# Optimization experiments

Measured on AMD Instinct MI355X. Metric: run time of the kernel, lower is better.

Reference implementation:

```python
import jax, jax.numpy as jnp
import numpy as np

EPSILON = 0.5

def setup_inputs() -> dict:
    key = jax.random.key(0)
    k1, k2, k3 = jax.random.split(key, 3)
    N, F, D = 8192, 128, 64
    X = jax.random.normal(k1, (N, F), dtype=jnp.float32)
    W_r = jax.random.normal(k2, (2 * F, D), dtype=jnp.float32)
    a_r = jax.random.normal(k3, (D,), dtype=jnp.float32)
    return {"X": X, "W_r": W_r, "a_r": a_r}

def reference(X, W_r, a_r):
    # Faithful to: cat(X_i, X_j) @ W_r @ a_r == (X @ W1 @ a_r)[i] + (X @ W2 @ a_r)[j]
    # (standard GAT decomposition -- avoids materializing [N, N, 2F]).
    F_ = X.shape[1]
    w1 = W_r[:F_] @ a_r          # [F]
    w2 = W_r[F_:] @ a_r          # [F]
    s1 = X @ w1                  # [N]
    s2 = X @ w2                  # [N]
    R = jax.nn.leaky_relu(s1[:, None] + s2[None, :])   # [N, N]
    # torch .std() is unbiased (ddof=1) over all elements
    R = (R - R.mean()) / (jnp.std(R, ddof=1) + 1e-5)
    E = jax.nn.softmax(R, axis=1)
    threshold = E.mean() / EPSILON
    filtered_E = jnp.where(E >= threshold, jnp.float32(1.0), jnp.float32(0.0))
    return filtered_E
```

## Files before the change

kernel.cpp:

```cpp
#include <hip/hip_runtime.h>
#include <math.h>

#define Nn 8192

static constexpr int S1o = 256;
static constexpr int S2o = S1o + Nn;
static constexpr int Mo  = S2o + Nn;
static constexpr int Zo  = Mo + Nn;
static constexpr int RRo = Zo + Nn;
static constexpr int STo = RRo + Nn;
static constexpr int RBo = STo + 8;

typedef float nfloat4 __attribute__((ext_vector_type(4)));

__device__ __forceinline__ float lrelu32(float z) {
    return (z >= 0.0f) ? z : __fmul_rn(0.01f, z);
}

__device__ __forceinline__ double exp_fast(double x) {
    x = fmin(fmax(x, -700.0), 700.0);
    const double INVLN2 = 1.44269504088896338700e+00;
    const double LN2HI  = 6.93147180369123816490e-01;
    const double LN2LO  = 1.90821492927058770002e-10;
    double nd = rint(x * INVLN2);
    double r  = fma(-nd, LN2HI, x);
    r = fma(-nd, LN2LO, r);
    double p = 1.56192069685862264622e-10;
    p = fma(p, r, 2.08767569878680989792e-09);
    p = fma(p, r, 2.50521083854417187751e-08);
    p = fma(p, r, 2.75573192239858906526e-07);
    p = fma(p, r, 2.75573192239858925110e-06);
    p = fma(p, r, 2.48015873015873015873e-05);
    p = fma(p, r, 1.98412698412698412698e-04);
    p = fma(p, r, 1.38888888888888894069e-03);
    p = fma(p, r, 8.33333333333333321769e-03);
    p = fma(p, r, 4.16666666666666643537e-02);
    p = fma(p, r, 1.66666666666666657415e-01);
    p = fma(p, r, 5.00000000000000000000e-01);
    p = fma(p, r, 1.0);
    p = fma(p, r, 1.0);
    long long n = (long long)nd;
    double sc = __longlong_as_double((n + 1023LL) << 52);
    return p * sc;
}
__device__ __forceinline__ float exp32cr(float x) {
    return (float)exp_fast((double)x);
}

__device__ float blas_dot(const float* __restrict__ a, const float* __restrict__ x, int n) {
    float lane[8];
#pragma unroll
    for (int l = 0; l < 8; ++l) lane[l] = 0.0f;
    for (int k = 0; k < n; k += 8) {
#pragma unroll
        for (int l = 0; l < 8; ++l) lane[l] = __fmaf_rn(a[k + l], x[k + l], lane[l]);
    }
    float s0 = __fadd_rn(lane[0], lane[4]);
    float s1 = __fadd_rn(lane[1], lane[5]);
    float s2 = __fadd_rn(lane[2], lane[6]);
    float s3 = __fadd_rn(lane[3], lane[7]);
    return __fadd_rn(__fadd_rn(s0, s1), __fadd_rn(s2, s3));
}

__device__ __forceinline__ unsigned f2key(float f) {
    unsigned u = __float_as_uint(f);
    return (u & 0x80000000u) ? ~u : (u | 0x80000000u);
}
__device__ __forceinline__ float key2f(unsigned k) {
    unsigned u = (k & 0x80000000u) ? (k & 0x7FFFFFFFu) : ~k;
    return __uint_as_float(u);
}

#define ROW_REDUCE_TAIL_SHFL(RESULT_STMT)                                     \
    {                                                                         \
        __syncthreads();                                                      \
        if (t < 64) {                                                         \
            float sl = __fadd_rn(__fadd_rn(red[t * 8 + 0], red[t * 8 + 1]),   \
                                 __fadd_rn(red[t * 8 + 2], red[t * 8 + 3]));  \
            float sr = __fadd_rn(__fadd_rn(red[t * 8 + 4], red[t * 8 + 5]),   \
                                 __fadd_rn(red[t * 8 + 6], red[t * 8 + 7]));  \
            float v = __fadd_rn(sl, sr);                                      \
            _Pragma("unroll") for (int s_ = 32; s_ >= 1; s_ >>= 1) {          \
                float a_ = __shfl(v, (2 * t) & 63);                           \
                float b_ = __shfl(v, (2 * t + 1) & 63);                       \
                if (t < s_) v = __fadd_rn(a_, b_);                            \
            }                                                                 \
            if (t == 0) { float total = v; RESULT_STMT; }                     \
        }                                                                     \
        __syncthreads();                                                      \
    }

#define GLOBAL_TREE_INPLACE(Abuf, NT, TOTALVAR)                               \
    {                                                                         \
        for (int s_ = 4096; s_ >= 1; s_ >>= 1) {                              \
            float v_[16];                                                     \
            int n_ = 0;                                                       \
            for (int idx = t; idx < s_; idx += NT)                            \
                v_[n_++] = __fadd_rn(Abuf[2 * idx], Abuf[2 * idx + 1]);       \
            __syncthreads();                                                  \
            n_ = 0;                                                           \
            for (int idx = t; idx < s_; idx += NT)                            \
                Abuf[idx] = v_[n_++];                                         \
            __syncthreads();                                                  \
        }                                                                     \
        TOTALVAR = Abuf[0];                                                   \
    }

__global__ __launch_bounds__(256) void k_s(const float* __restrict__ X,
                                           const float* __restrict__ Wr,
                                           const float* __restrict__ ar,
                                           float* __restrict__ scr) {
    __shared__ float w1[128], w2[128];
    int t = threadIdx.x;
    if (t < 128) {
        w1[t] = blas_dot(Wr + t * 64, ar, 64);
        w2[t] = blas_dot(Wr + (128 + t) * 64, ar, 64);
    }
    __syncthreads();
    int i = blockIdx.x * 256 + t;
    scr[S1o + i] = blas_dot(X + i * 128, w1, 128);
    scr[S2o + i] = blas_dot(X + i * 128, w2, 128);
}

__global__ __launch_bounds__(512) void k_stat0(const float* __restrict__ scr,
                                               float* __restrict__ rowredA) {
    __shared__ float red[512];
    int r0 = blockIdx.x * 16, t = threadIdx.x;
    int l = t >> 3, c = t & 7;
    const float* s2 = scr + S2o;
    int ebase = l * 128 + c;
    float sv[16];
#pragma unroll
    for (int k = 0; k < 16; ++k) sv[k] = s2[ebase + 8 * k];
    for (int rr = 0; rr < 16; ++rr) {
        float s1i = scr[S1o + r0 + rr];
        float r = lrelu32(__fadd_rn(s1i, sv[0]));
#pragma unroll
        for (int k = 1; k < 16; ++k)
            r = __fadd_rn(r, lrelu32(__fadd_rn(s1i, sv[k])));
        red[t] = r;
        ROW_REDUCE_TAIL_SHFL(rowredA[r0 + rr] = total)
    }
}

__global__ __launch_bounds__(512) void k_stat1(float* __restrict__ scr) {
    __shared__ float A[8192];
    __shared__ float red[512];
    int r0 = blockIdx.x * 16, t = threadIdx.x;
    const float* rowredA = scr + RRo;
    float* rowredB = scr + RBo;
    for (int idx = t; idx < 8192; idx += 512) A[idx] = rowredA[idx];
    __syncthreads();
    float total;
    GLOBAL_TREE_INPLACE(A, 512, total)
    float mu = __fdiv_rn(total, 67108864.0f);
    if (blockIdx.x == 0 && t == 0) scr[STo] = mu;

    int l = t >> 3, c = t & 7;
    const float* s2 = scr + S2o;
    int ebase = l * 128 + c;
    float sv[16];
#pragma unroll
    for (int k = 0; k < 16; ++k) sv[k] = s2[ebase + 8 * k];
    for (int rr = 0; rr < 16; ++rr) {
        float s1i = scr[S1o + r0 + rr];
        float d0 = __fsub_rn(lrelu32(__fadd_rn(s1i, sv[0])), mu);
        float r = __fmul_rn(d0, d0);
#pragma unroll
        for (int k = 1; k < 16; ++k) {
            float d = __fsub_rn(lrelu32(__fadd_rn(s1i, sv[k])), mu);
            r = __fadd_rn(r, __fmul_rn(d, d));
        }
        red[t] = r;
        ROW_REDUCE_TAIL_SHFL(rowredB[r0 + rr] = total)
    }
}

__global__ __launch_bounds__(1024) void k_tree_sig(const float* __restrict__ rowredB,
                                                   float* __restrict__ scr) {
    __shared__ float A[8192];
    __shared__ float B[4096];
    int t = threadIdx.x;
    for (int idx = t; idx < 8192; idx += 1024) A[idx] = rowredB[idx];
    __syncthreads();
    float* src = A;
    float* dst = B;
    for (int s = 4096; s >= 1; s >>= 1) {
        for (int idx = t; idx < s; idx += 1024)
            dst[idx] = __fadd_rn(src[2 * idx], src[2 * idx + 1]);
        __syncthreads();
        float* tmp = src; src = dst; dst = tmp;
    }
    if (t == 0) {
        float var = __fdiv_rn(src[0], 67108864.0f);
        scr[STo + 1] = __fadd_rn(__fsqrt_rn(var), 1e-5f);
    }
}

__global__ __launch_bounds__(512) void k_MZE2(float* __restrict__ scr) {
    __shared__ float red[512];
    __shared__ float wmax[8];
    __shared__ float Zsh;
    float* rowredE = scr + RRo;
    int t = threadIdx.x;
    int l = t >> 3, c = t & 7;
    const float* s2 = scr + S2o;
    float mu = scr[STo], sig = scr[STo + 1];
    int ebase = l * 128 + c;
    float sv[16];
#pragma unroll
    for (int k = 0; k < 16; ++k) sv[k] = s2[ebase + 8 * k];

    for (int rr = 0; rr < 2; ++rr) {
        int i = blockIdx.x * 2 + rr;
        float s1i = scr[S1o + i];

        float v[16];
        float mx = -3.4e38f;
#pragma unroll
        for (int k = 0; k < 16; ++k) {
            v[k] = __fdiv_rn(__fsub_rn(lrelu32(__fadd_rn(s1i, sv[k])), mu), sig);
            mx = fmaxf(mx, v[k]);
        }
#pragma unroll
        for (int o = 32; o > 0; o >>= 1) mx = fmaxf(mx, __shfl_xor(mx, o));
        if ((t & 63) == 0) wmax[t >> 6] = mx;
        __syncthreads();
        float Mi = fmaxf(fmaxf(fmaxf(wmax[0], wmax[1]), fmaxf(wmax[2], wmax[3])),
                         fmaxf(fmaxf(wmax[4], wmax[5]), fmaxf(wmax[6], wmax[7])));

        v[0] = exp32cr(__fsub_rn(v[0], Mi));
        float r = v[0];
#pragma unroll
        for (int k = 1; k < 16; ++k) {
            v[k] = exp32cr(__fsub_rn(v[k], Mi));
            r = __fadd_rn(r, v[k]);
        }
        red[t] = r;
        ROW_REDUCE_TAIL_SHFL(Zsh = total; scr[Zo + i] = total; scr[Mo + i] = Mi)
        float Zi = Zsh;

        float e = __fdiv_rn(v[0], Zi);
#pragma unroll
        for (int k = 1; k < 16; ++k)
            e = __fadd_rn(e, __fdiv_rn(v[k], Zi));
        red[t] = e;
        ROW_REDUCE_TAIL_SHFL(rowredE[i] = total)
    }
}

__global__ __launch_bounds__(256) void k_out(const float* __restrict__ scr,
                                             float* __restrict__ out) {
    __shared__ float A[8192];
    __shared__ unsigned kcut[8][3];
    int t = threadIdx.x;
    int r0 = blockIdx.x * 8;
    const float* rowredE = scr + RRo;
    for (int idx = t; idx < 8192; idx += 256) A[idx] = rowredE[idx];
    __syncthreads();
    float total;
    GLOBAL_TREE_INPLACE(A, 256, total)
    float mean = __fdiv_rn(total, 67108864.0f);
    float thr = __fdiv_rn(mean, 0.5f);
    float mu = scr[STo], sig = scr[STo + 1];

    if (t < 24) {
        int rr = t / 3, w = t - rr * 3;
        int i = r0 + rr;
        float s1i = scr[S1o + i];
        float Mi = scr[Mo + i], Zi = scr[Zo + i];
        double thr_d = (double)thr;
        unsigned lo = 0x00800000u;
        unsigned hi = 0xFF800000u;
        while (lo < hi) {
            unsigned mid = lo + ((hi - lo) >> 1);
            float s2v = key2f(mid);
            float Rn = __fdiv_rn(__fsub_rn(lrelu32(__fadd_rn(s1i, s2v)), mu), sig);
            float P = exp32cr(__fsub_rn(Rn, Mi));
            float E = __fdiv_rn(P, Zi);
            double m = ((double)E - thr_d) / thr_d;
            bool pred = (w == 0) ? (m >= -2.8e-8)
                      : (w == 1) ? (m > 2.8e-8)
                                 : (m >= 1.75e-7);
            if (pred) hi = mid; else lo = mid + 1;
        }
        kcut[rr][w] = lo;
    }
    __syncthreads();
    unsigned kA[8], kB[8], kC[8];
    long long rowbase[8];
#pragma unroll
    for (int rr = 0; rr < 8; ++rr) {
        kA[rr] = kcut[rr][0];
        kB[rr] = kcut[rr][1];
        kC[rr] = kcut[rr][2];
        rowbase[rr] = (long long)(r0 + rr) * Nn;
    }
    const float* s2 = scr + S2o;
    for (int ch = 0; ch < 8; ++ch) {
        int j0 = ch * 1024 + t * 4;
        nfloat4 sv = *reinterpret_cast<const nfloat4*>(s2 + j0);
        unsigned k0 = f2key(sv.x), k1 = f2key(sv.y), k2 = f2key(sv.z), k3 = f2key(sv.w);
#pragma unroll
        for (int rr = 0; rr < 8; ++rr) {
            unsigned a = kA[rr], b = kB[rr], cc = kC[rr];
            nfloat4 r;
            r.x = (k0 < a) ? 0.0f : (k0 < b) ? 1.0f : (k0 < cc) ? 0.0f : 1.0f;
            r.y = (k1 < a) ? 0.0f : (k1 < b) ? 1.0f : (k1 < cc) ? 0.0f : 1.0f;
            r.z = (k2 < a) ? 0.0f : (k2 < b) ? 1.0f : (k2 < cc) ? 0.0f : 1.0f;
            r.w = (k3 < a) ? 0.0f : (k3 < b) ? 1.0f : (k3 < cc) ? 0.0f : 1.0f;
            __builtin_nontemporal_store(r, reinterpret_cast<nfloat4*>(out + rowbase[rr] + j0));
        }
    }
}

extern "C" void kernel_launch(void* const* d_in, const int* in_sizes, int n_in,
                              void* d_out, int out_size, void* d_ws, size_t ws_size,
                              hipStream_t stream) {
    const float *X = nullptr, *Wr = nullptr, *ar = nullptr;
    for (int k = 0; k < n_in; ++k) {
        if      (in_sizes[k] == 1048576) X  = (const float*)d_in[k];
        else if (in_sizes[k] == 16384)   Wr = (const float*)d_in[k];
        else if (in_sizes[k] == 64)      ar = (const float*)d_in[k];
    }
    if (!X)  X  = (const float*)d_in[0];
    if (!Wr) Wr = (const float*)d_in[1];
    if (!ar) ar = (const float*)d_in[2];

    float* out = (float*)d_out;
    float* scr = (float*)d_ws;

    k_s        <<<32,   256, 0, stream>>>(X, Wr, ar, scr);
    k_stat0    <<<512,  512, 0, stream>>>(scr, scr + RRo);
    k_stat1    <<<512,  512, 0, stream>>>(scr);
    k_tree_sig <<<1,   1024, 0, stream>>>(scr + RBo, scr);
    k_MZE2     <<<4096, 512, 0, stream>>>(scr);
    k_out      <<<1024, 256, 0, stream>>>(scr, out);
}
```

Measured before the change: 209.0 us.

## Precompute row max analytically and hoist threshold reduction into single-block kernel

Each softmax row max is now derived from the global max of s2, because leaky ReLU and the normalisation are monotone. This removes a block-wide max reduction and one __syncthreads per row in k_MZE2, and it recomputes v instead of keeping it. The global sum of rowredE that every k_out block used to repeat over 8192 entries now runs once in a new k_tree_thr kernel, at the cost of one extra launch. The max is computed exactly, so results should match as long as monotonicity holds.

Result: no change. 209.8 us (+0.4%).

```diff
diff --git a/kernel.cpp b/kernel.cpp
--- a/kernel.cpp
+++ b/kernel.cpp
@@ -176,12 +176,19 @@
     }
 }
 
-__global__ __launch_bounds__(1024) void k_tree_sig(const float* __restrict__ rowredB,
-                                                   float* __restrict__ scr) {
+__global__ __launch_bounds__(1024) void k_tree_sig(float* __restrict__ scr) {
     __shared__ float A[8192];
     __shared__ float B[4096];
-    int t = threadIdx.x;
+    __shared__ float wm[16];
+    int t = threadIdx.x;
+    const float* rowredB = scr + RBo;
     for (int idx = t; idx < 8192; idx += 1024) A[idx] = rowredB[idx];
+    const float* s2 = scr + S2o;
+    float mx = -3.4e38f;
+    for (int idx = t; idx < 8192; idx += 1024) mx = fmaxf(mx, s2[idx]);
+#pragma unroll
+    for (int o = 32; o > 0; o >>= 1) mx = fmaxf(mx, __shfl_xor(mx, o));
+    if ((t & 63) == 0) wm[t >> 6] = mx;
     __syncthreads();
     float* src = A;
     float* dst = B;
@@ -194,18 +201,21 @@
     if (t == 0) {
         float var = __fdiv_rn(src[0], 67108864.0f);
         scr[STo + 1] = __fadd_rn(__fsqrt_rn(var), 1e-5f);
+        float m = wm[0];
+#pragma unroll
+        for (int k = 1; k < 16; ++k) m = fmaxf(m, wm[k]);
+        scr[STo + 3] = m;
     }
 }
 
 __global__ __launch_bounds__(512) void k_MZE2(float* __restrict__ scr) {
     __shared__ float red[512];
-    __shared__ float wmax[8];
     __shared__ float Zsh;
     float* rowredE = scr + RRo;
     int t = threadIdx.x;
     int l = t >> 3, c = t & 7;
     const float* s2 = scr + S2o;
-    float mu = scr[STo], sig = scr[STo + 1];
+    float mu = scr[STo], sig = scr[STo + 1], s2max = scr[STo + 3];
     int ebase = l * 128 + c;
     float sv[16];
 #pragma unroll
@@ -214,56 +224,58 @@
     for (int rr = 0; rr < 2; ++rr) {
         int i = blockIdx.x * 2 + rr;
         float s1i = scr[S1o + i];
-
-        float v[16];
-        float mx = -3.4e38f;
-#pragma unroll
-        for (int k = 0; k < 16; ++k) {
-            v[k] = __fdiv_rn(__fsub_rn(lrelu32(__fadd_rn(s1i, sv[k])), mu), sig);
-            mx = fmaxf(mx, v[k]);
-        }
-#pragma unroll
-        for (int o = 32; o > 0; o >>= 1) mx = fmaxf(mx, __shfl_xor(mx, o));
-        if ((t & 63) == 0) wmax[t >> 6] = mx;
-        __syncthreads();
-        float Mi = fmaxf(fmaxf(fmaxf(wmax[0], wmax[1]), fmaxf(wmax[2], wmax[3])),
-                         fmaxf(fmaxf(wmax[4], wmax[5]), fmaxf(wmax[6], wmax[7])));
-
-        v[0] = exp32cr(__fsub_rn(v[0], Mi));
-        float r = v[0];
+        float Mi = __fdiv_rn(__fsub_rn(lrelu32(__fadd_rn(s1i, s2max)), mu), sig);
+
+        float p[16];
+        p[0] = exp32cr(__fsub_rn(
+            __fdiv_rn(__fsub_rn(lrelu32(__fadd_rn(s1i, sv[0])), mu), sig), Mi));
+        float r = p[0];
 #pragma unroll
         for (int k = 1; k < 16; ++k) {
-            v[k] = exp32cr(__fsub_rn(v[k], Mi));
-            r = __fadd_rn(r, v[k]);
+            p[k] = exp32cr(__fsub_rn(
+                __fdiv_rn(__fsub_rn(lrelu32(__fadd_rn(s1i, sv[k])), mu), sig), Mi));
+            r = __fadd_rn(r, p[k]);
         }
         red[t] = r;
         ROW_REDUCE_TAIL_SHFL(Zsh = total; scr[Zo + i] = total; scr[Mo + i] = Mi)
         float Zi = Zsh;
 
-        float e = __fdiv_rn(v[0], Zi);
+        float e = __fdiv_rn(p[0], Zi);
 #pragma unroll
         for (int k = 1; k < 16; ++k)
-            e = __fadd_rn(e, __fdiv_rn(v[k], Zi));
+            e = __fadd_rn(e, __fdiv_rn(p[k], Zi));
         red[t] = e;
         ROW_REDUCE_TAIL_SHFL(rowredE[i] = total)
     }
 }
 
+__global__ __launch_bounds__(1024) void k_tree_thr(const float* __restrict__ rowredE,
+                                                   float* __restrict__ scr) {
+    __shared__ float A[8192];
+    __shared__ float B[4096];
+    int t = threadIdx.x;
+    for (int idx = t; idx < 8192; idx += 1024) A[idx] = rowredE[idx];
+    __syncthreads();
+    float* src = A;
+    float* dst = B;
+    for (int s = 4096; s >= 1; s >>= 1) {
+        for (int idx = t; idx < s; idx += 1024)
+            dst[idx] = __fadd_rn(src[2 * idx], src[2 * idx + 1]);
+        __syncthreads();
+        float* tmp = src; src = dst; dst = tmp;
+    }
+    if (t == 0) {
+        float mean = __fdiv_rn(src[0], 67108864.0f);
+        scr[STo + 2] = __fdiv_rn(mean, 0.5f);
+    }
+}
+
 __global__ __launch_bounds__(256) void k_out(const float* __restrict__ scr,
                                              float* __restrict__ out) {
-    __shared__ float A[8192];
     __shared__ unsigned kcut[8][3];
     int t = threadIdx.x;
     int r0 = blockIdx.x * 8;
-    const float* rowredE = scr + RRo;
-    for (int idx = t; idx < 8192; idx += 256) A[idx] = rowredE[idx];
-    __syncthreads();
-    float total;
-    GLOBAL_TREE_INPLACE(A, 256, total)
-    float mean = __fdiv_rn(total, 67108864.0f);
-    float thr = __fdiv_rn(mean, 0.5f);
-    float mu = scr[STo], sig = scr[STo + 1];
-
+    float mu = scr[STo], sig = scr[STo + 1], thr = scr[STo + 2];
     if (t < 24) {
         int rr = t / 3, w = t - rr * 3;
         int i = r0 + rr;
@@ -333,7 +345,8 @@
     k_s        <<<32,   256, 0, stream>>>(X, Wr, ar, scr);
     k_stat0    <<<512,  512, 0, stream>>>(scr, scr + RRo);
     k_stat1    <<<512,  512, 0, stream>>>(scr);
-    k_tree_sig <<<1,   1024, 0, stream>>>(scr + RBo, scr);
+    k_tree_sig <<<1,   1024, 0, stream>>>(scr);
     k_MZE2     <<<4096, 512, 0, stream>>>(scr);
+    k_tree_thr <<<1,   1024, 0, stream>>>(scr + RRo, scr);
     k_out      <<<1024, 256, 0, stream>>>(scr, out);
 }
```
